# Performance work log

Hardware: AMD Instinct MI355X
Metric: run time of the kernel (lower is better)

Reference implementation:

```python
import jax, jax.numpy as jnp
import numpy as np

B, S, H = 2, 1024, 2048          # batch, seq, hidden_size
I = 7168                          # intermediate_size
E = 8                             # num_local_experts
TOPK = 2                          # num_experts_per_tok
R = int(I * H * 0.1 / (I + H))    # delta_low_rank = 159


def setup_inputs() -> dict:
    key = jax.random.key(0)
    ks = jax.random.split(key, 12)
    s = 0.02
    return {
        "hidden_states": jax.random.normal(ks[0], (B, S, H), jnp.float32),
        "gate_w": jax.random.normal(ks[1], (E, H), jnp.float32) * s,
        "W1": jax.random.normal(ks[2], (E, I, H), jnp.float32) * s,
        "W2": jax.random.normal(ks[3], (E, H, I), jnp.float32) * s,
        "W3": jax.random.normal(ks[4], (E, I, H), jnp.float32) * s,
        "U1": jax.random.normal(ks[5], (E, I, R), jnp.float32) * s,
        "V1": jax.random.normal(ks[6], (E, R, H), jnp.float32) * s,
        "U2": jax.random.normal(ks[7], (E, H, R), jnp.float32) * s,
        "V2": jax.random.normal(ks[8], (E, R, I), jnp.float32) * s,
        "U3": jax.random.normal(ks[9], (E, I, R), jnp.float32) * s,
        "V3": jax.random.normal(ks[10], (E, R, H), jnp.float32) * s,
    }


def reference(hidden_states, gate_w, W1, W2, W3, U1, V1, U2, V2, U3, V3):
    b, s, h = hidden_states.shape
    x = hidden_states.reshape(-1, h)                     # [T, H]
    T = x.shape[0]
    router_logits = x @ gate_w.T                          # [T, E]
    probs = jax.nn.softmax(router_logits.astype(jnp.float32), axis=-1)
    rw, sel = jax.lax.top_k(probs, TOPK)                  # [T, k]
    rw = rw / jnp.sum(rw, axis=-1, keepdims=True)
    rw = rw.astype(x.dtype)
    # dense combine weights: zero for unselected experts (same math as gather/scatter)
    comb = jnp.zeros((T, E), x.dtype).at[jnp.arange(T)[:, None], sel].add(rw)
    out = jnp.zeros_like(x)
    for e in range(E):                                    # small fixed expert loop
        up = x @ W3[e].T + (x @ V3[e].T) @ U3[e].T        # [T, I]
        gate = x @ W1[e].T + (x @ V1[e].T) @ U1[e].T      # [T, I]
        hmid = jax.nn.silu(gate) * up                     # [T, I]
        y = hmid @ W2[e].T + (hmid @ V2[e].T) @ U2[e].T   # [T, H]
        out = out + comb[:, e, None] * y
    return out.reshape(b, s, h), router_logits
```

## Files before the change

kernel.cpp:

```cpp
#include <hip/hip_runtime.h>
#include <cstdint>
#include <cstddef>

#define TT 2048
#define HH 2048
#define II 7168
#define EE 8
#define RR 159
#define RPAD 192
#define ROWS 4096

typedef __attribute__((ext_vector_type(8))) short bf16x8;
typedef __attribute__((ext_vector_type(4))) short short4v;
typedef __attribute__((ext_vector_type(4))) float f32x4;

__device__ __forceinline__ unsigned short f2bf(float f) {
  unsigned int u = __float_as_uint(f);
  u += 0x7fffu + ((u >> 16) & 1u);
  return (unsigned short)(u >> 16);
}
__device__ __forceinline__ float bf2f(unsigned short u) {
  return __uint_as_float(((unsigned int)u) << 16);
}
__device__ __forceinline__ bf16x8 zero8() {
  bf16x8 v;
#pragma unroll
  for (int j = 0; j < 8; j++) v[j] = 0;
  return v;
}
__device__ __forceinline__ void gload16(const unsigned short* g, unsigned short* l) {
  __builtin_amdgcn_global_load_lds(
      (const __attribute__((address_space(1))) unsigned int*)g,
      (__attribute__((address_space(3))) unsigned int*)l, 16, 0, 0);
}

__global__ __launch_bounds__(256) void k_upad(const float* __restrict__ U,
                                              unsigned short* __restrict__ Up, int rows) {
  long long idx = (long long)blockIdx.x * 256 + threadIdx.x;
  long long total = (long long)rows * 24;
  if (idx >= total) return;
  int row = (int)(idx / 24), c8 = (int)(idx % 24);
  unsigned short* dp = Up + (size_t)row * RPAD + c8 * 8;
#pragma unroll
  for (int j = 0; j < 8; j++) {
    int c = c8 * 8 + j;
    dp[j] = (c < RR) ? f2bf(U[(size_t)row * RR + c]) : (unsigned short)0;
  }
}

__global__ __launch_bounds__(256, 2) void k_merge(
    const float* __restrict__ Wf, const unsigned short* __restrict__ Upad,
    const float* __restrict__ Vf, unsigned short* __restrict__ Wb,
    int M2, int C) {
  int e = blockIdx.z;
  int row0 = blockIdx.y * 128;
  int col0 = blockIdx.x * 128;
  const float* w = Wf + (size_t)e * M2 * C;
  const unsigned short* up = Upad + (size_t)e * M2 * RPAD;
  const float* vf = Vf + (size_t)e * RR * C;
  unsigned short* wb = Wb + (size_t)e * M2 * C;
  __shared__ unsigned short sbuf[17408];
  unsigned short* Us = sbuf;
  unsigned short* Vt = sbuf + 8192;
  unsigned short* Dl = sbuf;
  int tid = threadIdx.x, lane = tid & 63, wv = tid >> 6;
  int wr = (wv >> 1) * 64, wc = (wv & 1) * 64;
  int rstage = tid >> 3, cg = tid & 7;
  f32x4 acc[4][4];
#pragma unroll
  for (int m = 0; m < 4; m++)
#pragma unroll
    for (int n = 0; n < 4; n++) acc[m][n] = (f32x4){0.f, 0.f, 0.f, 0.f};
  int rl = tid & 15;
  int h8 = (tid >> 4) * 8;
  for (int kt = 0; kt < RPAD; kt += 64) {
#pragma unroll
    for (int p = 0; p < 4; p++) {
      int r = p * 32 + rstage;
      bf16x8 v = *(const bf16x8*)(up + (size_t)(row0 + r) * RPAD + kt + cg * 8);
      *(bf16x8*)&Us[r * 64 + ((cg ^ (r & 7)) * 8)] = v;
    }
#pragma unroll
    for (int rr = 0; rr < 4; rr++) {
      int r = rr * 16 + rl;
      int rg = kt + r;
      float4 a = {0, 0, 0, 0}, b = {0, 0, 0, 0};
      if (rg < RR) {
        a = *(const float4*)(vf + (size_t)rg * C + col0 + h8);
        b = *(const float4*)(vf + (size_t)rg * C + col0 + h8 + 4);
      }
      Vt[(h8 + 0) * 72 + r] = f2bf(a.x);
      Vt[(h8 + 1) * 72 + r] = f2bf(a.y);
      Vt[(h8 + 2) * 72 + r] = f2bf(a.z);
      Vt[(h8 + 3) * 72 + r] = f2bf(a.w);
      Vt[(h8 + 4) * 72 + r] = f2bf(b.x);
      Vt[(h8 + 5) * 72 + r] = f2bf(b.y);
      Vt[(h8 + 6) * 72 + r] = f2bf(b.z);
      Vt[(h8 + 7) * 72 + r] = f2bf(b.w);
    }
    __syncthreads();
#pragma unroll
    for (int ks = 0; ks < 2; ks++) {
      bf16x8 af[4], bf[4];
#pragma unroll
      for (int m = 0; m < 4; m++) {
        int r = wr + m * 16 + (lane & 15);
        af[m] = *(const bf16x8*)&Us[r * 64 + (((ks * 4 + (lane >> 4)) ^ (r & 7)) * 8)];
      }
#pragma unroll
      for (int n = 0; n < 4; n++) {
        int h = wc + n * 16 + (lane & 15);
        bf[n] = *(const bf16x8*)&Vt[h * 72 + (ks * 4 + (lane >> 4)) * 8];
      }
#pragma unroll
      for (int m = 0; m < 4; m++)
#pragma unroll
        for (int n = 0; n < 4; n++)
          acc[m][n] = __builtin_amdgcn_mfma_f32_16x16x32_bf16(af[m], bf[n], acc[m][n], 0, 0, 0);
    }
    __syncthreads();
  }
#pragma unroll
  for (int m = 0; m < 4; m++) {
#pragma unroll
    for (int r4 = 0; r4 < 4; r4++) {
      int row = wr + m * 16 + (lane >> 4) * 4 + r4;
#pragma unroll
      for (int n = 0; n < 4; n++) {
        int col = wc + n * 16 + (lane & 15);
        Dl[row * 136 + col] = f2bf(acc[m][n][r4]);
      }
    }
  }
  __syncthreads();
  {
    int rr = tid >> 5;
    int c4 = (tid & 31) * 4;
#pragma unroll
    for (int pass = 0; pass < 16; pass++) {
      int row = pass * 8 + rr;
      const float* src = w + (size_t)(row0 + row) * C + col0 + c4;
      float4 a = *(const float4*)src;
      const unsigned short* dl = &Dl[row * 136 + c4];
      short4v o;
      o[0] = (short)f2bf(a.x + bf2f(dl[0]));
      o[1] = (short)f2bf(a.y + bf2f(dl[1]));
      o[2] = (short)f2bf(a.z + bf2f(dl[2]));
      o[3] = (short)f2bf(a.w + bf2f(dl[3]));
      *(short4v*)(wb + (size_t)(row0 + row) * C + col0 + c4) = o;
    }
  }
}

__global__ __launch_bounds__(256) void k_router(
    const float* __restrict__ x, const float* __restrict__ gw,
    float* __restrict__ logits_out, int* __restrict__ sel,
    float* __restrict__ wtok, int* __restrict__ counts,
    unsigned short* __restrict__ xb) {
  int t = blockIdx.x;
  const float* xr = x + (size_t)t * HH;
  int base = threadIdx.x * 8;
  float4 x0 = *(const float4*)(xr + base);
  float4 x1 = *(const float4*)(xr + base + 4);
  {
    bf16x8 v;
    v[0] = (short)f2bf(x0.x); v[1] = (short)f2bf(x0.y);
    v[2] = (short)f2bf(x0.z); v[3] = (short)f2bf(x0.w);
    v[4] = (short)f2bf(x1.x); v[5] = (short)f2bf(x1.y);
    v[6] = (short)f2bf(x1.z); v[7] = (short)f2bf(x1.w);
    *(bf16x8*)(xb + (size_t)t * HH + base) = v;
  }
  float part[EE];
#pragma unroll
  for (int e = 0; e < EE; e++) {
    const float* g = gw + (size_t)e * HH + base;
    float4 g0 = *(const float4*)g;
    float4 g1 = *(const float4*)(g + 4);
    part[e] = x0.x * g0.x + x0.y * g0.y + x0.z * g0.z + x0.w * g0.w +
              x1.x * g1.x + x1.y * g1.y + x1.z * g1.z + x1.w * g1.w;
  }
#pragma unroll
  for (int off = 32; off > 0; off >>= 1)
#pragma unroll
    for (int e = 0; e < EE; e++) part[e] += __shfl_down(part[e], off);
  __shared__ float red[4][EE];
  int w = threadIdx.x >> 6, lane = threadIdx.x & 63;
  if (lane == 0) {
#pragma unroll
    for (int e = 0; e < EE; e++) red[w][e] = part[e];
  }
  __syncthreads();
  if (threadIdx.x == 0) {
    float lg[EE];
    float mx = -1e30f;
#pragma unroll
    for (int e = 0; e < EE; e++) {
      lg[e] = red[0][e] + red[1][e] + red[2][e] + red[3][e];
      logits_out[(size_t)t * EE + e] = lg[e];
      mx = fmaxf(mx, lg[e]);
    }
    float p[EE];
#pragma unroll
    for (int e = 0; e < EE; e++) p[e] = __expf(lg[e] - mx);
    int i0 = 0;
#pragma unroll
    for (int e = 1; e < EE; e++)
      if (lg[e] > lg[i0]) i0 = e;
    int i1 = (i0 == 0) ? 1 : 0;
#pragma unroll
    for (int e = 0; e < EE; e++)
      if (e != i0 && lg[e] > lg[i1]) i1 = e;
    float s = p[i0] + p[i1];
    sel[t * 2] = i0;
    sel[t * 2 + 1] = i1;
    wtok[t * 2] = p[i0] / s;
    wtok[t * 2 + 1] = p[i1] / s;
    atomicAdd(&counts[i0], 1);
    atomicAdd(&counts[i1], 1);
  }
}

__global__ void k_offsets(const int* __restrict__ counts, int* __restrict__ offs,
                          int* __restrict__ curs) {
  if (threadIdx.x == 0 && blockIdx.x == 0) {
    int o = 0;
    for (int e = 0; e < EE; e++) {
      offs[e] = o;
      curs[e] = o;
      o += counts[e];
    }
    offs[EE] = o;
  }
}

__global__ void k_build(const int* __restrict__ sel, const float* __restrict__ wtok,
                        int* __restrict__ curs, int* __restrict__ rowsA,
                        float* __restrict__ rowwgt, int* __restrict__ rowid) {
  int t = blockIdx.x * blockDim.x + threadIdx.x;
  if (t >= TT) return;
  for (int k = 0; k < 2; k++) {
    int e = sel[t * 2 + k];
    int pos = atomicAdd(&curs[e], 1);
    rowsA[pos] = t;
    rowwgt[pos] = wtok[t * 2 + k];
    rowid[t * 2 + k] = pos;
  }
}

__global__ __launch_bounds__(256, 2) void k_mlp1(
    const unsigned short* __restrict__ Xb,
    const unsigned short* __restrict__ W1b, const unsigned short* __restrict__ W3b,
    unsigned short* __restrict__ hmid,
    const int* __restrict__ counts, const int* __restrict__ offs,
    const int* __restrict__ rowsA) {
  int e = blockIdx.z;
  int cnt = counts[e];
  int m0 = blockIdx.y * 128;
  if (m0 >= cnt) return;
  int n0 = blockIdx.x * 128;
  int roff = offs[e];
  __shared__ unsigned short As[128 * 64];
  __shared__ unsigned short Bg[128 * 64];
  __shared__ unsigned short Bu[128 * 64];
  int tid = threadIdx.x, lane = tid & 63, w = tid >> 6;
  int wr = (w >> 1) * 64, wc = (w & 1) * 64;
  f32x4 accg[4][4], accu[4][4];
#pragma unroll
  for (int m = 0; m < 4; m++)
#pragma unroll
    for (int n = 0; n < 4; n++) {
      accg[m][n] = (f32x4){0.f, 0.f, 0.f, 0.f};
      accu[m][n] = (f32x4){0.f, 0.f, 0.f, 0.f};
    }
  int srow = (w << 5) + (lane >> 3);
  int swz = (((lane & 7) ^ ((lane >> 3) & 7)) << 3);
  const unsigned short* pa[4];
  const unsigned short* pg[4];
  const unsigned short* pu[4];
  {
    const unsigned short* w1 = W1b + (size_t)e * II * HH;
    const unsigned short* w3 = W3b + (size_t)e * II * HH;
#pragma unroll
    for (int i = 0; i < 4; i++) {
      int gr = m0 + srow + i * 8;
      if (gr >= cnt) gr = cnt - 1;
      pa[i] = Xb + (size_t)rowsA[roff + gr] * HH + swz;
      pg[i] = w1 + (size_t)(n0 + srow + i * 8) * HH + swz;
      pu[i] = w3 + (size_t)(n0 + srow + i * 8) * HH + swz;
    }
  }
  for (int kt = 0; kt < HH; kt += 64) {
#pragma unroll
    for (int i = 0; i < 4; i++) {
      gload16(pa[i] + kt, &As[((w << 5) + (i << 3)) * 64]);
      gload16(pg[i] + kt, &Bg[((w << 5) + (i << 3)) * 64]);
      gload16(pu[i] + kt, &Bu[((w << 5) + (i << 3)) * 64]);
    }
    __syncthreads();
#pragma unroll
    for (int ks = 0; ks < 2; ks++) {
      bf16x8 af[4], bg[4], bu[4];
#pragma unroll
      for (int m = 0; m < 4; m++) {
        int r = wr + m * 16 + (lane & 15);
        af[m] = *(const bf16x8*)&As[r * 64 + (((ks * 4 + (lane >> 4)) ^ (r & 7)) * 8)];
      }
#pragma unroll
      for (int n = 0; n < 4; n++) {
        int r = wc + n * 16 + (lane & 15);
        int idx = r * 64 + (((ks * 4 + (lane >> 4)) ^ (r & 7)) * 8);
        bg[n] = *(const bf16x8*)&Bg[idx];
        bu[n] = *(const bf16x8*)&Bu[idx];
      }
#pragma unroll
      for (int m = 0; m < 4; m++)
#pragma unroll
        for (int n = 0; n < 4; n++) {
          accg[m][n] = __builtin_amdgcn_mfma_f32_16x16x32_bf16(af[m], bg[n], accg[m][n], 0, 0, 0);
          accu[m][n] = __builtin_amdgcn_mfma_f32_16x16x32_bf16(af[m], bu[n], accu[m][n], 0, 0, 0);
        }
    }
    __syncthreads();
  }
#pragma unroll
  for (int m = 0; m < 4; m++) {
#pragma unroll
    for (int r4 = 0; r4 < 4; r4++) {
      int row = m0 + wr + m * 16 + (lane >> 4) * 4 + r4;
      if (row < cnt) {
        size_t rb = (size_t)(roff + row) * II + n0 + wc;
#pragma unroll
        for (int n = 0; n < 4; n++) {
          float g = accg[m][n][r4], uu = accu[m][n][r4];
          float h = (g / (1.f + __expf(-g))) * uu;
          hmid[rb + n * 16 + (lane & 15)] = f2bf(h);
        }
      }
    }
  }
}

__global__ __launch_bounds__(256, 2) void k_mlp2(
    const unsigned short* __restrict__ hmid,
    const unsigned short* __restrict__ W2b,
    const float* __restrict__ rowwgt, float* __restrict__ ybuf,
    const int* __restrict__ counts, const int* __restrict__ offs) {
  int e = blockIdx.z;
  int cnt = counts[e];
  int m0 = blockIdx.y * 128;
  if (m0 >= cnt) return;
  int n0 = blockIdx.x * 128;
  int roff = offs[e];
  __shared__ unsigned short As[128 * 64];
  __shared__ unsigned short Bs[128 * 64];
  int tid = threadIdx.x, lane = tid & 63, w = tid >> 6;
  int wr = (w >> 1) * 64, wc = (w & 1) * 64;
  f32x4 acc[4][4];
#pragma unroll
  for (int m = 0; m < 4; m++)
#pragma unroll
    for (int n = 0; n < 4; n++) acc[m][n] = (f32x4){0.f, 0.f, 0.f, 0.f};
  int srow = (w << 5) + (lane >> 3);
  int swz = (((lane & 7) ^ ((lane >> 3) & 7)) << 3);
  const unsigned short* pa[4];
  const unsigned short* pb[4];
  {
    const unsigned short* w2 = W2b + (size_t)e * HH * II;
#pragma unroll
    for (int i = 0; i < 4; i++) {
      int gr = m0 + srow + i * 8;
      if (gr >= cnt) gr = cnt - 1;
      pa[i] = hmid + (size_t)(roff + gr) * II + swz;
      pb[i] = w2 + (size_t)(n0 + srow + i * 8) * II + swz;
    }
  }
  for (int kt = 0; kt < II; kt += 64) {
#pragma unroll
    for (int i = 0; i < 4; i++) {
      gload16(pa[i] + kt, &As[((w << 5) + (i << 3)) * 64]);
      gload16(pb[i] + kt, &Bs[((w << 5) + (i << 3)) * 64]);
    }
    __syncthreads();
#pragma unroll
    for (int ks = 0; ks < 2; ks++) {
      bf16x8 af[4], bs[4];
#pragma unroll
      for (int m = 0; m < 4; m++) {
        int r = wr + m * 16 + (lane & 15);
        af[m] = *(const bf16x8*)&As[r * 64 + (((ks * 4 + (lane >> 4)) ^ (r & 7)) * 8)];
      }
#pragma unroll
      for (int n = 0; n < 4; n++) {
        int r = wc + n * 16 + (lane & 15);
        bs[n] = *(const bf16x8*)&Bs[r * 64 + (((ks * 4 + (lane >> 4)) ^ (r & 7)) * 8)];
      }
#pragma unroll
      for (int m = 0; m < 4; m++)
#pragma unroll
        for (int n = 0; n < 4; n++)
          acc[m][n] = __builtin_amdgcn_mfma_f32_16x16x32_bf16(af[m], bs[n], acc[m][n], 0, 0, 0);
    }
    __syncthreads();
  }
#pragma unroll
  for (int m = 0; m < 4; m++) {
#pragma unroll
    for (int r4 = 0; r4 < 4; r4++) {
      int row = m0 + wr + m * 16 + (lane >> 4) * 4 + r4;
      if (row < cnt) {
        float wgt = rowwgt[roff + row];
        size_t rb = (size_t)(roff + row) * HH + n0 + wc;
#pragma unroll
        for (int n = 0; n < 4; n++)
          ybuf[rb + n * 16 + (lane & 15)] = acc[m][n][r4] * wgt;
      }
    }
  }
}

__global__ void k_combine(const float* __restrict__ ybuf, const int* __restrict__ rowid,
                          float* __restrict__ out) {
  int idx = blockIdx.x * 256 + threadIdx.x;
  int t = idx >> 8;
  int c = (idx & 255) * 8;
  int r0 = rowid[t * 2], r1 = rowid[t * 2 + 1];
  const float* y0 = ybuf + (size_t)r0 * HH + c;
  const float* y1 = ybuf + (size_t)r1 * HH + c;
  float4 a0 = *(const float4*)y0, a1 = *(const float4*)(y0 + 4);
  float4 b0 = *(const float4*)y1, b1 = *(const float4*)(y1 + 4);
  float4 o0 = {a0.x + b0.x, a0.y + b0.y, a0.z + b0.z, a0.w + b0.w};
  float4 o1 = {a1.x + b1.x, a1.y + b1.y, a1.z + b1.z, a1.w + b1.w};
  float* o = out + (size_t)t * HH + c;
  *(float4*)o = o0;
  *(float4*)(o + 4) = o1;
}

extern "C" void kernel_launch(void* const* d_in, const int* in_sizes, int n_in,
                              void* d_out, int out_size, void* d_ws, size_t ws_size,
                              hipStream_t stream) {
  const float* x  = (const float*)d_in[0];
  const float* gw = (const float*)d_in[1];
  const float* W1 = (const float*)d_in[2];
  const float* W2 = (const float*)d_in[3];
  const float* W3 = (const float*)d_in[4];
  const float* U1 = (const float*)d_in[5];
  const float* V1 = (const float*)d_in[6];
  const float* U2 = (const float*)d_in[7];
  const float* V2 = (const float*)d_in[8];
  const float* U3 = (const float*)d_in[9];
  const float* V3 = (const float*)d_in[10];
  float* out = (float*)d_out;
  float* logits = out + (size_t)TT * HH;

  char* ws = (char*)d_ws;
  size_t off = 0;
  auto take = [&](size_t b) -> char* {
    char* p = ws + off;
    off += (b + 255) & ~(size_t)255;
    return p;
  };
  unsigned short* Xb   = (unsigned short*)take((size_t)TT * HH * 2);
  unsigned short* hmid = (unsigned short*)take((size_t)ROWS * II * 2);
  float* ybuf          = (float*)take((size_t)ROWS * HH * 4);
  int* sel             = (int*)take((size_t)TT * 2 * 4);
  float* wtok          = (float*)take((size_t)TT * 2 * 4);
  int* rowsA           = (int*)take((size_t)ROWS * 4);
  float* rowwgt        = (float*)take((size_t)ROWS * 4);
  int* rowid           = (int*)take((size_t)TT * 2 * 4);
  int* meta            = (int*)take(1024);
  int* counts  = meta;
  int* offs    = meta + 16;
  int* curs    = meta + 32;
  unsigned short* W1b = (unsigned short*)take((size_t)EE * II * HH * 2);
  unsigned short* W3b = (unsigned short*)take((size_t)EE * II * HH * 2);
  unsigned short* W2b = (unsigned short*)take((size_t)EE * HH * II * 2);
  unsigned short* U1p = (unsigned short*)take((size_t)EE * II * RPAD * 2);
  unsigned short* U3p = (unsigned short*)take((size_t)EE * II * RPAD * 2);
  unsigned short* U2p = (unsigned short*)take((size_t)EE * HH * RPAD * 2);

  hipMemsetAsync(counts, 0, EE * sizeof(int), stream);
  k_upad<<<(EE * II * 24 + 255) / 256, 256, 0, stream>>>(U1, U1p, EE * II);
  k_upad<<<(EE * II * 24 + 255) / 256, 256, 0, stream>>>(U3, U3p, EE * II);
  k_upad<<<(EE * HH * 24 + 255) / 256, 256, 0, stream>>>(U2, U2p, EE * HH);
  k_merge<<<dim3(HH / 128, II / 128, EE), 256, 0, stream>>>(W1, U1p, V1, W1b, II, HH);
  k_merge<<<dim3(HH / 128, II / 128, EE), 256, 0, stream>>>(W3, U3p, V3, W3b, II, HH);
  k_merge<<<dim3(II / 128, HH / 128, EE), 256, 0, stream>>>(W2, U2p, V2, W2b, HH, II);
  k_router<<<TT, 256, 0, stream>>>(x, gw, logits, sel, wtok, counts, Xb);
  k_offsets<<<1, 64, 0, stream>>>(counts, offs, curs);
  k_build<<<TT / 256, 256, 0, stream>>>(sel, wtok, curs, rowsA, rowwgt, rowid);
  k_mlp1<<<dim3(II / 128, TT / 128, EE), 256, 0, stream>>>(
      Xb, W1b, W3b, hmid, counts, offs, rowsA);
  k_mlp2<<<dim3(HH / 128, TT / 128, EE), 256, 0, stream>>>(
      hmid, W2b, rowwgt, ybuf, counts, offs);
  k_combine<<<(TT * HH / 8) / 256, 256, 0, stream>>>(ybuf, rowid, out);
}
```

Before: 1.197 ms.

## Pre-transpose V to bf16 and stage merge tiles with async global-to-LDS loads

Adds a k_vt pre-pass that converts each V matrix to bf16 and transposes it into a padded [C, RPAD] layout. k_merge can then stage both the U and V tiles with direct 16-byte global-to-LDS loads into a shared XOR-swizzled layout, replacing the per-element fp32 convert and scattered transposing LDS stores. The launch-bounds occupancy hint rises from 2 to 4, and the epilogue loop is split into chunks so fewer loads are unrolled at once. The cost is an extra kernel pass over V, extra scratch buffers, and possible register pressure at the higher occupancy target.

```diff
diff --git a/kernel.cpp b/kernel.cpp
--- a/kernel.cpp
+++ b/kernel.cpp
@@ -48,55 +48,61 @@
   }
 }
 
-__global__ __launch_bounds__(256, 2) void k_merge(
+__global__ __launch_bounds__(256) void k_vt(const float* __restrict__ V,
+                                            unsigned short* __restrict__ Vt, int C) {
+  int e = blockIdx.y;
+  int h = blockIdx.x * 64 + (threadIdx.x & 63);
+  int q = threadIdx.x >> 6;
+  const float* v = V + (size_t)e * RR * C + h;
+  unsigned short* o = Vt + ((size_t)e * C + h) * RPAD;
+  for (int g = 0; g < 6; g++) {
+    int r0 = q * 48 + g * 8;
+    bf16x8 pk;
+#pragma unroll
+    for (int j = 0; j < 8; j++) {
+      int r = r0 + j;
+      pk[j] = (short)((r < RR) ? f2bf(v[(size_t)r * C]) : (unsigned short)0);
+    }
+    *(bf16x8*)(o + r0) = pk;
+  }
+}
+
+__global__ __launch_bounds__(256, 4) void k_merge(
     const float* __restrict__ Wf, const unsigned short* __restrict__ Upad,
-    const float* __restrict__ Vf, unsigned short* __restrict__ Wb,
+    const unsigned short* __restrict__ Vtg, unsigned short* __restrict__ Wb,
     int M2, int C) {
   int e = blockIdx.z;
   int row0 = blockIdx.y * 128;
   int col0 = blockIdx.x * 128;
   const float* w = Wf + (size_t)e * M2 * C;
   const unsigned short* up = Upad + (size_t)e * M2 * RPAD;
-  const float* vf = Vf + (size_t)e * RR * C;
+  const unsigned short* vt = Vtg + (size_t)e * C * RPAD;
   unsigned short* wb = Wb + (size_t)e * M2 * C;
   __shared__ unsigned short sbuf[17408];
   unsigned short* Us = sbuf;
-  unsigned short* Vt = sbuf + 8192;
+  unsigned short* Vs = sbuf + 8192;
   unsigned short* Dl = sbuf;
   int tid = threadIdx.x, lane = tid & 63, wv = tid >> 6;
   int wr = (wv >> 1) * 64, wc = (wv & 1) * 64;
-  int rstage = tid >> 3, cg = tid & 7;
   f32x4 acc[4][4];
 #pragma unroll
   for (int m = 0; m < 4; m++)
 #pragma unroll
     for (int n = 0; n < 4; n++) acc[m][n] = (f32x4){0.f, 0.f, 0.f, 0.f};
-  int rl = tid & 15;
-  int h8 = (tid >> 4) * 8;
+  int srow = (wv << 5) + (lane >> 3);
+  int swz = (((lane & 7) ^ ((lane >> 3) & 7)) << 3);
+  const unsigned short* pu[4];
+  const unsigned short* pv[4];
+#pragma unroll
+  for (int i = 0; i < 4; i++) {
+    pu[i] = up + (size_t)(row0 + srow + i * 8) * RPAD + swz;
+    pv[i] = vt + (size_t)(col0 + srow + i * 8) * RPAD + swz;
+  }
   for (int kt = 0; kt < RPAD; kt += 64) {
 #pragma unroll
-    for (int p = 0; p < 4; p++) {
-      int r = p * 32 + rstage;
-      bf16x8 v = *(const bf16x8*)(up + (size_t)(row0 + r) * RPAD + kt + cg * 8);
-      *(bf16x8*)&Us[r * 64 + ((cg ^ (r & 7)) * 8)] = v;
-    }
-#pragma unroll
-    for (int rr = 0; rr < 4; rr++) {
-      int r = rr * 16 + rl;
-      int rg = kt + r;
-      float4 a = {0, 0, 0, 0}, b = {0, 0, 0, 0};
-      if (rg < RR) {
-        a = *(const float4*)(vf + (size_t)rg * C + col0 + h8);
-        b = *(const float4*)(vf + (size_t)rg * C + col0 + h8 + 4);
-      }
-      Vt[(h8 + 0) * 72 + r] = f2bf(a.x);
-      Vt[(h8 + 1) * 72 + r] = f2bf(a.y);
-      Vt[(h8 + 2) * 72 + r] = f2bf(a.z);
-      Vt[(h8 + 3) * 72 + r] = f2bf(a.w);
-      Vt[(h8 + 4) * 72 + r] = f2bf(b.x);
-      Vt[(h8 + 5) * 72 + r] = f2bf(b.y);
-      Vt[(h8 + 6) * 72 + r] = f2bf(b.z);
-      Vt[(h8 + 7) * 72 + r] = f2bf(b.w);
+    for (int i = 0; i < 4; i++) {
+      gload16(pu[i] + kt, &Us[((wv << 5) + (i << 3)) * 64]);
+      gload16(pv[i] + kt, &Vs[((wv << 5) + (i << 3)) * 64]);
     }
     __syncthreads();
 #pragma unroll
@@ -109,8 +115,8 @@
       }
 #pragma unroll
       for (int n = 0; n < 4; n++) {
-        int h = wc + n * 16 + (lane & 15);
-        bf[n] = *(const bf16x8*)&Vt[h * 72 + (ks * 4 + (lane >> 4)) * 8];
+        int r = wc + n * 16 + (lane & 15);
+        bf[n] = *(const bf16x8*)&Vs[r * 64 + (((ks * 4 + (lane >> 4)) ^ (r & 7)) * 8)];
       }
 #pragma unroll
       for (int m = 0; m < 4; m++)
@@ -136,18 +142,20 @@
   {
     int rr = tid >> 5;
     int c4 = (tid & 31) * 4;
-#pragma unroll
-    for (int pass = 0; pass < 16; pass++) {
-      int row = pass * 8 + rr;
-      const float* src = w + (size_t)(row0 + row) * C + col0 + c4;
-      float4 a = *(const float4*)src;
-      const unsigned short* dl = &Dl[row * 136 + c4];
-      short4v o;
-      o[0] = (short)f2bf(a.x + bf2f(dl[0]));
-      o[1] = (short)f2bf(a.y + bf2f(dl[1]));
-      o[2] = (short)f2bf(a.z + bf2f(dl[2]));
-      o[3] = (short)f2bf(a.w + bf2f(dl[3]));
-      *(short4v*)(wb + (size_t)(row0 + row) * C + col0 + c4) = o;
+    for (int pc = 0; pc < 4; pc++) {
+#pragma unroll
+      for (int p = 0; p < 4; p++) {
+        int row = (pc * 4 + p) * 8 + rr;
+        const float* src = w + (size_t)(row0 + row) * C + col0 + c4;
+        float4 a = *(const float4*)src;
+        const unsigned short* dl = &Dl[row * 136 + c4];
+        short4v o;
+        o[0] = (short)f2bf(a.x + bf2f(dl[0]));
+        o[1] = (short)f2bf(a.y + bf2f(dl[1]));
+        o[2] = (short)f2bf(a.z + bf2f(dl[2]));
+        o[3] = (short)f2bf(a.w + bf2f(dl[3]));
+        *(short4v*)(wb + (size_t)(row0 + row) * C + col0 + c4) = o;
+      }
     }
   }
 }
@@ -474,6 +482,9 @@
   unsigned short* W1b = (unsigned short*)take((size_t)EE * II * HH * 2);
   unsigned short* W3b = (unsigned short*)take((size_t)EE * II * HH * 2);
   unsigned short* W2b = (unsigned short*)take((size_t)EE * HH * II * 2);
+  unsigned short* V1t = (unsigned short*)take((size_t)EE * HH * RPAD * 2);
+  unsigned short* V3t = (unsigned short*)take((size_t)EE * HH * RPAD * 2);
+  unsigned short* V2t = (unsigned short*)take((size_t)EE * II * RPAD * 2);
   unsigned short* U1p = (unsigned short*)take((size_t)EE * II * RPAD * 2);
   unsigned short* U3p = (unsigned short*)take((size_t)EE * II * RPAD * 2);
   unsigned short* U2p = (unsigned short*)take((size_t)EE * HH * RPAD * 2);
@@ -482,9 +493,12 @@
   k_upad<<<(EE * II * 24 + 255) / 256, 256, 0, stream>>>(U1, U1p, EE * II);
   k_upad<<<(EE * II * 24 + 255) / 256, 256, 0, stream>>>(U3, U3p, EE * II);
   k_upad<<<(EE * HH * 24 + 255) / 256, 256, 0, stream>>>(U2, U2p, EE * HH);
-  k_merge<<<dim3(HH / 128, II / 128, EE), 256, 0, stream>>>(W1, U1p, V1, W1b, II, HH);
-  k_merge<<<dim3(HH / 128, II / 128, EE), 256, 0, stream>>>(W3, U3p, V3, W3b, II, HH);
-  k_merge<<<dim3(II / 128, HH / 128, EE), 256, 0, stream>>>(W2, U2p, V2, W2b, HH, II);
+  k_vt<<<dim3(HH / 64, EE), 256, 0, stream>>>(V1, V1t, HH);
+  k_vt<<<dim3(HH / 64, EE), 256, 0, stream>>>(V3, V3t, HH);
+  k_vt<<<dim3(II / 64, EE), 256, 0, stream>>>(V2, V2t, II);
+  k_merge<<<dim3(HH / 128, II / 128, EE), 256, 0, stream>>>(W1, U1p, V1t, W1b, II, HH);
+  k_merge<<<dim3(HH / 128, II / 128, EE), 256, 0, stream>>>(W3, U3p, V3t, W3b, II, HH);
+  k_merge<<<dim3(II / 128, HH / 128, EE), 256, 0, stream>>>(W2, U2p, V2t, W2b, HH, II);
   k_router<<<TT, 256, 0, stream>>>(x, gw, logits, sel, wtok, counts, Xb);
   k_offsets<<<1, 64, 0, stream>>>(counts, offs, curs);
   k_build<<<TT / 256, 256, 0, stream>>>(sel, wtok, curs, rowsA, rowwgt, rowid);
```

Result: no change. 1.189 ms (-0.7%).
